# Optimization experiments

Hardware: AMD Instinct MI355X
Metric: run time of the kernel (lower is better)

Reference implementation:

```python
import jax, jax.numpy as jnp
import numpy as np

DIM = 512
NUM_HEADS = 8
HEAD_DIM = DIM // NUM_HEADS
MAX_SLICES = 1024
SCALE = float(np.sqrt(HEAD_DIM))


def setup_inputs() -> dict:
    key = jax.random.key(0)
    ks = jax.random.split(key, 12)
    B, Nv, Nt, D = 4, 1024, 512, DIM
    std = 0.02
    inp = {
        "visual_tokens": jax.random.normal(ks[0], (B, Nv, D), jnp.float32),
        "text_tokens": jax.random.normal(ks[1], (B, Nt, D), jnp.float32),
        # Linear weights stored as [in, out] (i.e., torch W^T), so y = x @ W + b
        "W_Q": jax.random.normal(ks[2], (D, D), jnp.float32) * std,
        "b_Q": jnp.zeros((D,), jnp.float32),
        "W_K": jax.random.normal(ks[3], (D, D), jnp.float32) * std,
        "b_K": jnp.zeros((D,), jnp.float32),
        "W_V": jax.random.normal(ks[4], (D, D), jnp.float32) * std,
        "b_V": jnp.zeros((D,), jnp.float32),
        "W_O": jax.random.normal(ks[5], (D, D), jnp.float32) * std,
        "b_O": jnp.zeros((D,), jnp.float32),
        "bias_table": jax.random.normal(ks[6], (2 * MAX_SLICES - 1, NUM_HEADS), jnp.float32) * std,
        "ln_gamma": jnp.ones((D,), jnp.float32),
        "ln_beta": jnp.zeros((D,), jnp.float32),
    }
    return inp


def _layernorm(x, gamma, beta, eps=1e-5):
    mu = jnp.mean(x, axis=-1, keepdims=True)
    var = jnp.var(x, axis=-1, keepdims=True)
    return (x - mu) * jax.lax.rsqrt(var + eps) * gamma + beta


def reference(visual_tokens, text_tokens, W_Q, b_Q, W_K, b_K, W_V, b_V, W_O, b_O,
              bias_table, ln_gamma, ln_beta):
    Z = jnp.concatenate([visual_tokens, text_tokens], axis=1)  # [B, N, D]
    B, N, D = Z.shape
    Z = _layernorm(Z, ln_gamma, ln_beta)

    def proj(W, b):
        return (Z @ W + b).reshape(B, N, NUM_HEADS, HEAD_DIM).transpose(0, 2, 1, 3)

    Q = proj(W_Q, b_Q)  # [B, H, N, hd]
    K = proj(W_K, b_K)
    V = proj(W_V, b_V)

    attn = jnp.einsum("bhqd,bhkd->bhqk", Q, K) / SCALE  # [B, H, N, N]

    # relative slice bias: [H, N, N]
    coords = jnp.arange(N)
    rel = coords[:, None] - coords[None, :] + (MAX_SLICES - 1)
    rel = jnp.clip(rel, 0, 2 * MAX_SLICES - 2)
    bias = bias_table[rel]                      # [N, N, H]
    bias = jnp.transpose(bias, (2, 0, 1))[None]  # [1, H, N, N]

    attn = jax.nn.softmax(attn + bias, axis=-1)
    out = jnp.einsum("bhqk,bhkd->bhqd", attn, V)  # [B, H, N, hd]
    out = out.transpose(0, 2, 1, 3).reshape(B, N, D)
    return out @ W_O + b_O
```

## Files before the change

### kernel.cpp

```cpp
#include <hip/hip_runtime.h>
#include <stdint.h>

#define NSEQ   1536
#define NBATCH 4
#define NM     (NBATCH * NSEQ)
#define DMODEL 512
#define NHEAD  8
#define HD     64
#define TBLN   2047

typedef __attribute__((ext_vector_type(4))) float  f32x4;
typedef __attribute__((ext_vector_type(4))) int    i32x4;
typedef __attribute__((ext_vector_type(8))) __bf16 bf16x8;
typedef unsigned short u16;

static_assert(sizeof(bf16x8) == 16, "bf16x8 must be 16B");

__device__ inline u16 f2bf(float f) {
  union { float f; uint32_t u; } v; v.f = f;
  uint32_t u = v.u;
  return (u16)((u + 0x7fffu + ((u >> 16) & 1u)) >> 16);
}

__device__ inline bf16x8 ld_bf8(const u16* p) {
  i32x4 v = *(const i32x4*)p;
  return __builtin_bit_cast(bf16x8, v);
}

__device__ inline f32x4 mfma16(bf16x8 a, bf16x8 b, f32x4 c) {
  return __builtin_amdgcn_mfma_f32_16x16x32_bf16(a, b, c, 0, 0, 0);
}

__device__ inline void gload_lds16(const void* g, void* l) {
  __builtin_amdgcn_global_load_lds(
      (__attribute__((address_space(1))) void*)(g),
      (__attribute__((address_space(3))) void*)(l), 16, 0, 0);
}

__device__ inline uint32_t pkbf(float a, float b) {
  uint32_t r;
  asm("v_cvt_pk_bf16_f32 %0, %1, %2" : "=v"(r) : "v"(a), "v"(b));
  return r;
}

__device__ inline float exp2_raw(float x) {
  float r;
  asm("v_exp_f32 %0, %1" : "=v"(r) : "v"(x));
  return r;
}

__device__ inline float bfhi(uint32_t u) {
  union { uint32_t u; float f; } v; v.u = u & 0xffff0000u; return v.f;
}
__device__ inline float bflo(uint32_t u) {
  union { uint32_t u; float f; } v; v.u = u << 16; return v.f;
}

__global__ __launch_bounds__(256) void ln_kernel(
    const float* __restrict__ vis, const float* __restrict__ txt,
    const float* __restrict__ gamma, const float* __restrict__ beta,
    u16* __restrict__ zn) {
  const int lane = threadIdx.x & 63;
  const int row  = blockIdx.x * 4 + (threadIdx.x >> 6);
  const int b = row / NSEQ, n = row - b * NSEQ;
  const float* src = (n < 1024) ? (vis + ((size_t)b * 1024 + n) * DMODEL)
                                : (txt + ((size_t)b * 512 + (n - 1024)) * DMODEL);
  const float4* s4 = (const float4*)src;
  float4 x0 = s4[lane], x1 = s4[lane + 64];
  float s = x0.x + x0.y + x0.z + x0.w + x1.x + x1.y + x1.z + x1.w;
  float q = x0.x*x0.x + x0.y*x0.y + x0.z*x0.z + x0.w*x0.w
          + x1.x*x1.x + x1.y*x1.y + x1.z*x1.z + x1.w*x1.w;
  #pragma unroll
  for (int m = 1; m < 64; m <<= 1) { s += __shfl_xor(s, m); q += __shfl_xor(q, m); }
  const float mean = s * (1.0f / 512.0f);
  const float var  = q * (1.0f / 512.0f) - mean * mean;
  const float rstd = rsqrtf(var + 1e-5f);
  const float4* g4 = (const float4*)gamma;
  const float4* b4 = (const float4*)beta;
  float4 g0 = g4[lane], g1 = g4[lane + 64], p0 = b4[lane], p1 = b4[lane + 64];
  u16* dst = zn + (size_t)row * DMODEL;
  ushort4 o0, o1;
  o0.x = f2bf((x0.x - mean) * rstd * g0.x + p0.x);
  o0.y = f2bf((x0.y - mean) * rstd * g0.y + p0.y);
  o0.z = f2bf((x0.z - mean) * rstd * g0.z + p0.z);
  o0.w = f2bf((x0.w - mean) * rstd * g0.w + p0.w);
  o1.x = f2bf((x1.x - mean) * rstd * g1.x + p1.x);
  o1.y = f2bf((x1.y - mean) * rstd * g1.y + p1.y);
  o1.z = f2bf((x1.z - mean) * rstd * g1.z + p1.z);
  o1.w = f2bf((x1.w - mean) * rstd * g1.w + p1.w);
  *(ushort4*)(dst + lane * 4)        = o0;
  *(ushort4*)(dst + (lane + 64) * 4) = o1;
}

__global__ __launch_bounds__(256) void wtrans_kernel(
    const float* __restrict__ WQ, const float* __restrict__ WK,
    const float* __restrict__ WV, const float* __restrict__ WO,
    u16* __restrict__ wqkvt, u16* __restrict__ wot) {
  __shared__ float t[32][33];
  const int m = blockIdx.z;
  const float* W = (m == 0) ? WQ : (m == 1) ? WK : (m == 2) ? WV : WO;
  const int n0 = blockIdx.x * 32, k0 = blockIdx.y * 32;
  const int tx = threadIdx.x & 31, ty = threadIdx.x >> 5;
  #pragma unroll
  for (int j = 0; j < 4; ++j)
    t[ty + j * 8][tx] = W[(size_t)(k0 + ty + j * 8) * DMODEL + n0 + tx];
  __syncthreads();
  u16* out = (m < 3) ? (wqkvt + (size_t)m * DMODEL * DMODEL) : wot;
  #pragma unroll
  for (int j = 0; j < 4; ++j)
    out[(size_t)(n0 + ty + j * 8) * DMODEL + k0 + tx] = f2bf(t[tx][ty + j * 8]);
}

__global__ __launch_bounds__(256) void gemm_qkv(
    const u16* __restrict__ A, const u16* __restrict__ Bt,
    const float* __restrict__ bQ, const float* __restrict__ bK, const float* __restrict__ bV,
    u16* __restrict__ Q, u16* __restrict__ Kk, u16* __restrict__ Vt) {
  __shared__ __align__(16) u16 lat[128 * 64];
  __shared__ __align__(16) u16 lbt[96 * 64];
  const int tid = threadIdx.x, lane = tid & 63, w = tid >> 6;
  const int wr = w >> 1, wc = w & 1;
  const int m0 = blockIdx.y * 128, n0 = blockIdx.x * 96;
  f32x4 acc[4][3] = {};
  for (int kt = 0; kt < 8; ++kt) {
    const int k0 = kt * 64;
    #pragma unroll
    for (int i = 0; i < 4; ++i) {
      int ch = tid + 256 * i;
      int row = ch >> 3, pc = ch & 7;
      int kk = k0 + ((pc ^ (row & 7)) << 3);
      gload_lds16(A + (size_t)(m0 + row) * DMODEL + kk, lat + (size_t)ch * 8);
    }
    #pragma unroll
    for (int i = 0; i < 3; ++i) {
      int ch = tid + 256 * i;
      int row = ch >> 3, pc = ch & 7;
      int kk = k0 + ((pc ^ (row & 7)) << 3);
      gload_lds16(Bt + (size_t)(n0 + row) * DMODEL + kk, lbt + (size_t)ch * 8);
    }
    __syncthreads();
    #pragma unroll
    for (int ks = 0; ks < 2; ++ks) {
      bf16x8 af[4], bfr[3];
      const int cc = ks * 4 + (lane >> 4);
      #pragma unroll
      for (int f = 0; f < 4; ++f) {
        int ra = wr * 64 + f * 16 + (lane & 15);
        af[f]  = ld_bf8(lat + ra * 64 + ((cc ^ (ra & 7)) << 3));
      }
      #pragma unroll
      for (int f = 0; f < 3; ++f) {
        int rb = wc * 48 + f * 16 + (lane & 15);
        bfr[f] = ld_bf8(lbt + rb * 64 + ((cc ^ (rb & 7)) << 3));
      }
      #pragma unroll
      for (int fr = 0; fr < 4; ++fr)
        #pragma unroll
        for (int fc = 0; fc < 3; ++fc)
          acc[fr][fc] = mfma16(af[fr], bfr[fc], acc[fr][fc]);
    }
    __syncthreads();
  }
  #pragma unroll
  for (int fr = 0; fr < 4; ++fr) {
    const int mbase = m0 + wr * 64 + fr * 16 + ((lane >> 4) << 2);
    const int b = mbase / NSEQ;
    const int nseq = mbase - b * NSEQ;
    #pragma unroll
    for (int fc = 0; fc < 3; ++fc) {
      const int col = n0 + wc * 48 + fc * 16 + (lane & 15);
      const int which = col >> 9;
      const int cw = col & 511;
      const int h = cw >> 6, d = cw & 63;
      const float bias = (which == 0) ? bQ[cw] : (which == 1) ? bK[cw] : bV[cw];
      if (which < 2) {
        u16* dst = ((which == 0) ? Q : Kk) + ((size_t)(b * NHEAD + h) * NSEQ + nseq) * HD + d;
        #pragma unroll
        for (int r = 0; r < 4; ++r) dst[(size_t)r * HD] = f2bf(acc[fr][fc][r] + bias);
      } else {
        ushort4 pv;
        pv.x = f2bf(acc[fr][fc][0] + bias);
        pv.y = f2bf(acc[fr][fc][1] + bias);
        pv.z = f2bf(acc[fr][fc][2] + bias);
        pv.w = f2bf(acc[fr][fc][3] + bias);
        *(ushort4*)(Vt + ((size_t)(b * NHEAD + h) * HD + d) * NSEQ + nseq) = pv;
      }
    }
  }
}

__global__ __launch_bounds__(256) void gemm_oproj(
    const u16* __restrict__ A, const u16* __restrict__ Bt,
    const float* __restrict__ bO, float* __restrict__ out) {
  __shared__ __align__(16) u16 lat[64 * 64];
  __shared__ __align__(16) u16 lbt[64 * 64];
  const int tid = threadIdx.x, lane = tid & 63, w = tid >> 6;
  const int wr = w >> 1, wc = w & 1;
  const int m0 = blockIdx.y * 64, n0 = blockIdx.x * 64;
  f32x4 acc[2][2] = {};
  for (int kt = 0; kt < 8; ++kt) {
    const int k0 = kt * 64;
    #pragma unroll
    for (int i = 0; i < 2; ++i) {
      int ch = tid + 256 * i;
      int row = ch >> 3, pc = ch & 7;
      int kk = k0 + ((pc ^ (row & 7)) << 3);
      gload_lds16(A  + (size_t)(m0 + row) * DMODEL + kk, lat + (size_t)ch * 8);
      gload_lds16(Bt + (size_t)(n0 + row) * DMODEL + kk, lbt + (size_t)ch * 8);
    }
    __syncthreads();
    #pragma unroll
    for (int ks = 0; ks < 2; ++ks) {
      bf16x8 af[2], bfr[2];
      const int cc = ks * 4 + (lane >> 4);
      #pragma unroll
      for (int f = 0; f < 2; ++f) {
        int ra = wr * 32 + f * 16 + (lane & 15);
        af[f]  = ld_bf8(lat + ra * 64 + ((cc ^ (ra & 7)) << 3));
        int rb = wc * 32 + f * 16 + (lane & 15);
        bfr[f] = ld_bf8(lbt + rb * 64 + ((cc ^ (rb & 7)) << 3));
      }
      #pragma unroll
      for (int fr = 0; fr < 2; ++fr)
        #pragma unroll
        for (int fc = 0; fc < 2; ++fc)
          acc[fr][fc] = mfma16(af[fr], bfr[fc], acc[fr][fc]);
    }
    __syncthreads();
  }
  #pragma unroll
  for (int fr = 0; fr < 2; ++fr) {
    const int mbase = m0 + wr * 32 + fr * 16 + ((lane >> 4) << 2);
    #pragma unroll
    for (int fc = 0; fc < 2; ++fc) {
      const int col = n0 + wc * 32 + fc * 16 + (lane & 15);
      const float bias = bO[col];
      float* dst = out + (size_t)mbase * DMODEL + col;
      #pragma unroll
      for (int r = 0; r < 4; ++r) dst[(size_t)r * DMODEL] = acc[fr][fc][r] + bias;
    }
  }
}

__global__ __launch_bounds__(512, 1) void attn_kernel(
    const u16* __restrict__ Q, const u16* __restrict__ K,
    const u16* __restrict__ Vt, const float* __restrict__ table,
    u16* __restrict__ O) {
  __shared__ __align__(16) char smem[126976];
  u16* rb2k = (u16*)smem;
  const int tid = threadIdx.x, lane = tid & 63, w = tid >> 6;
  const int bid = blockIdx.x;
  const int xcd = bid & 7, idx = bid >> 3;
  const int bh  = xcd * 4 + (idx & 3);
  const int qt  = idx >> 2;
  const int h   = bh & (NHEAD - 1);
  for (int t = tid; t < 2 * 3072; t += 512) {
    const int c = (t >= 3072) ? 1 : 0;
    const int x = t - c * 3072;
    int src = 2558 - (x + c);
    src = src < 0 ? 0 : (src > 2046 ? 2046 : src);
    rb2k[c * 3072 + x] = f2bf(table[(size_t)src * NHEAD + h] * 1.4426950408889634f);
  }

  const int lo16 = lane & 15, g = lane >> 4;
  const int ws = w & 3;
  const int hf = w >> 2;
  const int kbase = hf * 768;
  const int q0 = qt * 192 + ws * 48;
  const u16* Qb = Q  + (size_t)bh * NSEQ * HD;
  const u16* Kb = K  + (size_t)bh * NSEQ * HD;
  const u16* Vb = Vt + (size_t)bh * HD * NSEQ;

  const int tloc = tid & 255, shf = tid >> 8;
  const int skbase = shf * 768;
  u16* kl0 = (u16*)(smem + 12288) + shf * 2 * 4096;
  u16* vl0 = (u16*)(smem + 45056) + shf * 2 * 4096;
#define STAGE(b, k0loc)                                                       \
  do {                                                                        \
    _Pragma("unroll")                                                         \
    for (int i = 0; i < 2; ++i) {                                             \
      int ch = tloc + 256 * i;                                                \
      int row = ch >> 3, pc = ch & 7;                                         \
      int col = (pc ^ (row & 7)) << 3;                                        \
      gload_lds16(Kb + (size_t)(skbase + (k0loc) + row) * HD + col,           \
                  kl0 + (size_t)(b) * 4096 + ch * 8);                         \
      gload_lds16(Vb + (size_t)row * NSEQ + skbase + (k0loc) + col,           \
                  vl0 + (size_t)(b) * 4096 + ch * 8);                         \
    }                                                                         \
  } while (0)

  bf16x8 qf[3][2];
  #pragma unroll
  for (int s = 0; s < 3; ++s)
    #pragma unroll
    for (int kd = 0; kd < 2; ++kd)
      qf[s][kd] = ld_bf8(Qb + (size_t)(q0 + s * 16 + lo16) * HD + kd * 32 + g * 8);

  float l_part[3] = {0.f, 0.f, 0.f};
  f32x4 acc[3][4] = {};

  char* plb = smem + 77824 + w * 6144;
  const int pswz  = (lo16 & 7) << 4;
  const int wbase = lo16 * 128;
  const int rswz  = lo16 & 7;
  const int B   = 1535 - q0 - lo16 + 4 * g - 32;
  const int c2  = B & 1;
  const int dwb = (B - c2) >> 1;
  const uint32_t* rbp32 = (const uint32_t*)(rb2k + c2 * 3072);
  const float c1 = 0.125f * 1.4426950408889634f;

  STAGE(0, 0);
  __syncthreads();
  int cur = 0;

  for (int kt = 0; kt < 12; ++kt) {
    const int kglob = kbase + kt * 64;
    const int nxt = cur ^ 1;
    if (kt < 11) {
      STAGE(nxt, (kt + 1) * 64);
      asm volatile("s_waitcnt vmcnt(4)" ::: "memory");
    } else {
      asm volatile("s_waitcnt vmcnt(0)" ::: "memory");
    }
    __builtin_amdgcn_s_barrier();
    const u16* kb = (u16*)(smem + 12288) + (hf * 2 + cur) * 4096;
    const u16* vb = (u16*)(smem + 45056) + (hf * 2 + cur) * 4096;
    float bvf[6][4];
    #pragma unroll
    for (int j = 0; j < 6; ++j) {
      const uint32_t u0 = rbp32[dwb + (kglob >> 1) + 8 * j];
      const uint32_t u1 = rbp32[dwb + (kglob >> 1) + 8 * j + 1];
      bvf[j][0] = bflo(u0); bvf[j][1] = bfhi(u0);
      bvf[j][2] = bflo(u1); bvf[j][3] = bfhi(u1);
    }
    f32x4 st[3][4] = {};
    __builtin_amdgcn_s_setprio(1);
    #pragma unroll
    for (int kc = 0; kc < 4; ++kc) {
      const int row = kc * 16 + lo16;
      const bf16x8 kf0 = ld_bf8(kb + row * 64 + ((g ^ rswz) << 3));
      const bf16x8 kf1 = ld_bf8(kb + row * 64 + (((4 + g) ^ rswz) << 3));
      #pragma unroll
      for (int s = 0; s < 3; ++s) {
        st[s][kc] = mfma16(kf0, qf[s][0], st[s][kc]);
        st[s][kc] = mfma16(kf1, qf[s][1], st[s][kc]);
      }
    }
    __builtin_amdgcn_s_setprio(0);
    #pragma unroll
    for (int s = 0; s < 3; ++s) {
      char* pls = plb + s * 2048;
      #pragma unroll
      for (int kc = 0; kc < 4; ++kc) {
        #pragma unroll
        for (int r = 0; r < 4; ++r) {
          float p = exp2_raw(__builtin_fmaf(st[s][kc][r], c1, bvf[kc - s + 2][r]));
          st[s][kc][r] = p;
          l_part[s] += p;
        }
        uint2 pr;
        pr.x = pkbf(st[s][kc][0], st[s][kc][1]);
        pr.y = pkbf(st[s][kc][2], st[s][kc][3]);
        *(uint2*)(pls + wbase + ((kc * 32 + g * 8) ^ pswz)) = pr;
      }
    }
    __builtin_amdgcn_s_setprio(1);
    #pragma unroll
    for (int t = 0; t < 2; ++t) {
      bf16x8 pb[3];
      #pragma unroll
      for (int s = 0; s < 3; ++s)
        pb[s] = ld_bf8((const u16*)(plb + s * 2048 + wbase + ((t * 64 + g * 16) ^ pswz)));
      #pragma unroll
      for (int fc = 0; fc < 4; ++fc) {
        const int row = fc * 16 + lo16;
        const bf16x8 vf = ld_bf8(vb + row * 64 + (((t * 4 + g) ^ rswz) << 3));
        #pragma unroll
        for (int s = 0; s < 3; ++s)
          acc[s][fc] = mfma16(vf, pb[s], acc[s][fc]);
      }
    }
    __builtin_amdgcn_s_setprio(0);
    __builtin_amdgcn_s_barrier();
    cur = nxt;
  }
  float* scr = (float*)(smem + 12288);
  if (hf == 1) {
    float* wb = scr + ws * 3264;
    #pragma unroll
    for (int s = 0; s < 3; ++s) {
      #pragma unroll
      for (int fc = 0; fc < 4; ++fc)
        ((f32x4*)wb)[(s * 4 + fc) * 64 + lane] = acc[s][fc];
      wb[3072 + s * 64 + lane] = l_part[s];
    }
  }
  __syncthreads();
  if (hf == 0) {
    const float* rb = scr + ws * 3264;
    #pragma unroll
    for (int s = 0; s < 3; ++s) {
      #pragma unroll
      for (int fc = 0; fc < 4; ++fc)
        acc[s][fc] += ((const f32x4*)rb)[(s * 4 + fc) * 64 + lane];
      l_part[s] += rb[3072 + s * 64 + lane];
    }
    const int b = bh >> 3;
    #pragma unroll
    for (int s = 0; s < 3; ++s) {
      float l_r = l_part[s];
      l_r += __shfl_xor(l_r, 16);
      l_r += __shfl_xor(l_r, 32);
      const float inv = 1.0f / l_r;
      u16* orow = O + ((size_t)(b * NSEQ + q0 + s * 16 + lo16)) * DMODEL + h * HD;
      #pragma unroll
      for (int fc = 0; fc < 4; ++fc) {
        uint2 o4;
        o4.x = pkbf(acc[s][fc][0] * inv, acc[s][fc][1] * inv);
        o4.y = pkbf(acc[s][fc][2] * inv, acc[s][fc][3] * inv);
        *(uint2*)(orow + fc * 16 + g * 4) = o4;
      }
    }
  }
#undef STAGE
}

extern "C" void kernel_launch(void* const* d_in, const int* in_sizes, int n_in,
                              void* d_out, int out_size, void* d_ws, size_t ws_size,
                              hipStream_t stream) {
  const float* vis   = (const float*)d_in[0];
  const float* txt   = (const float*)d_in[1];
  const float* WQ    = (const float*)d_in[2];
  const float* bQ    = (const float*)d_in[3];
  const float* WK    = (const float*)d_in[4];
  const float* bK    = (const float*)d_in[5];
  const float* WV    = (const float*)d_in[6];
  const float* bV    = (const float*)d_in[7];
  const float* WO    = (const float*)d_in[8];
  const float* bO    = (const float*)d_in[9];
  const float* table = (const float*)d_in[10];
  const float* gamma = (const float*)d_in[11];
  const float* beta  = (const float*)d_in[12];
  float* out = (float*)d_out;

  char* p = (char*)d_ws;
  u16* zn    = (u16*)p; p += (size_t)NM * DMODEL * 2;
  u16* wqkvt = (u16*)p; p += (size_t)3 * DMODEL * DMODEL * 2;
  u16* wot   = (u16*)p; p += (size_t)DMODEL * DMODEL * 2;
  u16* q     = (u16*)p; p += (size_t)NM * DMODEL * 2;
  u16* k     = (u16*)p; p += (size_t)NM * DMODEL * 2;
  u16* vt    = (u16*)p; p += (size_t)NM * DMODEL * 2;
  u16* o     = (u16*)p; p += (size_t)NM * DMODEL * 2;

  hipLaunchKernelGGL(ln_kernel, dim3(NM / 4), dim3(256), 0, stream,
                     vis, txt, gamma, beta, zn);
  hipLaunchKernelGGL(wtrans_kernel, dim3(16, 16, 4), dim3(256), 0, stream,
                     WQ, WK, WV, WO, wqkvt, wot);
  hipLaunchKernelGGL(gemm_qkv, dim3(16, 48), dim3(256), 0, stream,
                     zn, wqkvt, bQ, bK, bV, q, k, vt);
  hipLaunchKernelGGL(attn_kernel, dim3(256), dim3(512), 0, stream,
                     q, k, vt, table, o);
  hipLaunchKernelGGL(gemm_oproj, dim3(8, 96), dim3(256), 0, stream,
                     o, wot, bO, out);
}
```

Measured before the change: 82.45 us.

## Switch attention to 32x32 MFMA with register-resident P via permlane swaps

The attention kernel moves from 16x16x32 to 32x32x16 bf16 MFMA tiles, with each warp owning 32 query rows instead of 48. The softmax probabilities stay in registers and are rearranged into the B-operand layout with permlane32 swaps, which drops the per-warp LDS staging buffer for P. The block grows to 12 warps (768 threads) and shared memory shrinks from about 124KB to 76KB. The costs are fewer queries per warp, idle warps during staging, and higher register pressure under the new launch bounds.

```diff
diff --git a/kernel.cpp b/kernel.cpp
--- a/kernel.cpp
+++ b/kernel.cpp
@@ -9,9 +9,11 @@
 #define HD     64
 #define TBLN   2047
 
-typedef __attribute__((ext_vector_type(4))) float  f32x4;
-typedef __attribute__((ext_vector_type(4))) int    i32x4;
-typedef __attribute__((ext_vector_type(8))) __bf16 bf16x8;
+typedef __attribute__((ext_vector_type(4)))  float f32x4;
+typedef __attribute__((ext_vector_type(16))) float f32x16;
+typedef __attribute__((ext_vector_type(4)))  int   i32x4;
+typedef __attribute__((ext_vector_type(2)))  unsigned u32x2;
+typedef __attribute__((ext_vector_type(8)))  __bf16 bf16x8;
 typedef unsigned short u16;
 
 static_assert(sizeof(bf16x8) == 16, "bf16x8 must be 16B");
@@ -31,6 +33,10 @@
   return __builtin_amdgcn_mfma_f32_16x16x32_bf16(a, b, c, 0, 0, 0);
 }
 
+__device__ inline f32x16 mfma32(bf16x8 a, bf16x8 b, f32x16 c) {
+  return __builtin_amdgcn_mfma_f32_32x32x16_bf16(a, b, c, 0, 0, 0);
+}
+
 __device__ inline void gload_lds16(const void* g, void* l) {
   __builtin_amdgcn_global_load_lds(
       (__attribute__((address_space(1))) void*)(g),
@@ -41,6 +47,19 @@
   uint32_t r;
   asm("v_cvt_pk_bf16_f32 %0, %1, %2" : "=v"(r) : "v"(a), "v"(b));
   return r;
+}
+
+__device__ inline void plswap(uint32_t& a, uint32_t& b, int hi) {
+#if __has_builtin(__builtin_amdgcn_permlane32_swap)
+  u32x2 r = __builtin_amdgcn_permlane32_swap(a, b, false, false);
+  a = r[0]; b = r[1];
+#else
+  const uint32_t as = (uint32_t)__shfl_xor((int)a, 32);
+  const uint32_t bs = (uint32_t)__shfl_xor((int)b, 32);
+  const uint32_t na = hi ? bs : a;
+  const uint32_t nb = hi ? b : as;
+  a = na; b = nb;
+#endif
 }
 
 __device__ inline float exp2_raw(float x) {
@@ -241,11 +260,11 @@
   }
 }
 
-__global__ __launch_bounds__(512, 1) void attn_kernel(
+__global__ __launch_bounds__(768, 3) void attn_kernel(
     const u16* __restrict__ Q, const u16* __restrict__ K,
     const u16* __restrict__ Vt, const float* __restrict__ table,
     u16* __restrict__ O) {
-  __shared__ __align__(16) char smem[126976];
+  __shared__ __align__(16) char smem[77824];
   u16* rb2k = (u16*)smem;
   const int tid = threadIdx.x, lane = tid & 63, w = tid >> 6;
   const int bid = blockIdx.x;
@@ -253,7 +272,7 @@
   const int bh  = xcd * 4 + (idx & 3);
   const int qt  = idx >> 2;
   const int h   = bh & (NHEAD - 1);
-  for (int t = tid; t < 2 * 3072; t += 512) {
+  for (int t = tid; t < 2 * 3072; t += 768) {
     const int c = (t >= 3072) ? 1 : 0;
     const int x = t - c * 3072;
     int src = 2558 - (x + c);
@@ -261,50 +280,44 @@
     rb2k[c * 3072 + x] = f2bf(table[(size_t)src * NHEAD + h] * 1.4426950408889634f);
   }
 
-  const int lo16 = lane & 15, g = lane >> 4;
-  const int ws = w & 3;
-  const int hf = w >> 2;
+  const int lo32 = lane & 31, hi = lane >> 5;
+  const int ws = (w < 6) ? w : (w - 6);
+  const int hf = (w < 6) ? 0 : 1;
   const int kbase = hf * 768;
-  const int q0 = qt * 192 + ws * 48;
+  const int q  = qt * 192 + ws * 32 + lo32;
   const u16* Qb = Q  + (size_t)bh * NSEQ * HD;
   const u16* Kb = K  + (size_t)bh * NSEQ * HD;
   const u16* Vb = Vt + (size_t)bh * HD * NSEQ;
 
-  const int tloc = tid & 255, shf = tid >> 8;
-  const int skbase = shf * 768;
-  u16* kl0 = (u16*)(smem + 12288) + shf * 2 * 4096;
-  u16* vl0 = (u16*)(smem + 45056) + shf * 2 * 4096;
+  const int tloc = tid - hf * 384;
+  u16* kl0 = (u16*)(smem + 12288) + hf * 2 * 4096;
+  u16* vl0 = (u16*)(smem + 45056) + hf * 2 * 4096;
 #define STAGE(b, k0loc)                                                       \
-  do {                                                                        \
+  if (tloc < 256) {                                                           \
     _Pragma("unroll")                                                         \
     for (int i = 0; i < 2; ++i) {                                             \
       int ch = tloc + 256 * i;                                                \
       int row = ch >> 3, pc = ch & 7;                                         \
       int col = (pc ^ (row & 7)) << 3;                                        \
-      gload_lds16(Kb + (size_t)(skbase + (k0loc) + row) * HD + col,           \
+      gload_lds16(Kb + (size_t)(kbase + (k0loc) + row) * HD + col,            \
                   kl0 + (size_t)(b) * 4096 + ch * 8);                         \
-      gload_lds16(Vb + (size_t)row * NSEQ + skbase + (k0loc) + col,           \
+      gload_lds16(Vb + (size_t)row * NSEQ + kbase + (k0loc) + col,            \
                   vl0 + (size_t)(b) * 4096 + ch * 8);                         \
     }                                                                         \
-  } while (0)
-
-  bf16x8 qf[3][2];
-  #pragma unroll
-  for (int s = 0; s < 3; ++s)
-    #pragma unroll
-    for (int kd = 0; kd < 2; ++kd)
-      qf[s][kd] = ld_bf8(Qb + (size_t)(q0 + s * 16 + lo16) * HD + kd * 32 + g * 8);
-
-  float l_part[3] = {0.f, 0.f, 0.f};
-  f32x4 acc[3][4] = {};
-
-  char* plb = smem + 77824 + w * 6144;
-  const int pswz  = (lo16 & 7) << 4;
-  const int wbase = lo16 * 128;
-  const int rswz  = lo16 & 7;
-  const int B   = 1535 - q0 - lo16 + 4 * g - 32;
-  const int c2  = B & 1;
-  const int dwb = (B - c2) >> 1;
+  }
+
+  bf16x8 qf[4];
+  #pragma unroll
+  for (int ds = 0; ds < 4; ++ds)
+    qf[ds] = ld_bf8(Qb + (size_t)q * HD + ds * 16 + hi * 8);
+
+  float l_part = 0.f;
+  f32x16 acc[2] = {};
+
+  const int rswz = lo32 & 7;
+  const int T0  = 1535 - q + 4 * hi + kbase;
+  const int c2  = T0 & 1;
+  const int dwb = (T0 - c2) >> 1;
   const uint32_t* rbp32 = (const uint32_t*)(rb2k + c2 * 3072);
   const float c1 = 0.125f * 1.4426950408889634f;
 
@@ -313,7 +326,6 @@
   int cur = 0;
 
   for (int kt = 0; kt < 12; ++kt) {
-    const int kglob = kbase + kt * 64;
     const int nxt = cur ^ 1;
     if (kt < 11) {
       STAGE(nxt, (kt + 1) * 64);
@@ -324,102 +336,93 @@
     __builtin_amdgcn_s_barrier();
     const u16* kb = (u16*)(smem + 12288) + (hf * 2 + cur) * 4096;
     const u16* vb = (u16*)(smem + 45056) + (hf * 2 + cur) * 4096;
-    float bvf[6][4];
-    #pragma unroll
-    for (int j = 0; j < 6; ++j) {
-      const uint32_t u0 = rbp32[dwb + (kglob >> 1) + 8 * j];
-      const uint32_t u1 = rbp32[dwb + (kglob >> 1) + 8 * j + 1];
-      bvf[j][0] = bflo(u0); bvf[j][1] = bfhi(u0);
-      bvf[j][2] = bflo(u1); bvf[j][3] = bfhi(u1);
-    }
-    f32x4 st[3][4] = {};
-    __builtin_amdgcn_s_setprio(1);
-    #pragma unroll
-    for (int kc = 0; kc < 4; ++kc) {
-      const int row = kc * 16 + lo16;
-      const bf16x8 kf0 = ld_bf8(kb + row * 64 + ((g ^ rswz) << 3));
-      const bf16x8 kf1 = ld_bf8(kb + row * 64 + (((4 + g) ^ rswz) << 3));
-      #pragma unroll
-      for (int s = 0; s < 3; ++s) {
-        st[s][kc] = mfma16(kf0, qf[s][0], st[s][kc]);
-        st[s][kc] = mfma16(kf1, qf[s][1], st[s][kc]);
-      }
-    }
-    __builtin_amdgcn_s_setprio(0);
-    #pragma unroll
-    for (int s = 0; s < 3; ++s) {
-      char* pls = plb + s * 2048;
-      #pragma unroll
-      for (int kc = 0; kc < 4; ++kc) {
-        #pragma unroll
-        for (int r = 0; r < 4; ++r) {
-          float p = exp2_raw(__builtin_fmaf(st[s][kc][r], c1, bvf[kc - s + 2][r]));
-          st[s][kc][r] = p;
-          l_part[s] += p;
-        }
-        uint2 pr;
-        pr.x = pkbf(st[s][kc][0], st[s][kc][1]);
-        pr.y = pkbf(st[s][kc][2], st[s][kc][3]);
-        *(uint2*)(pls + wbase + ((kc * 32 + g * 8) ^ pswz)) = pr;
-      }
-    }
-    __builtin_amdgcn_s_setprio(1);
-    #pragma unroll
-    for (int t = 0; t < 2; ++t) {
-      bf16x8 pb[3];
-      #pragma unroll
-      for (int s = 0; s < 3; ++s)
-        pb[s] = ld_bf8((const u16*)(plb + s * 2048 + wbase + ((t * 64 + g * 16) ^ pswz)));
-      #pragma unroll
-      for (int fc = 0; fc < 4; ++fc) {
-        const int row = fc * 16 + lo16;
-        const bf16x8 vf = ld_bf8(vb + row * 64 + (((t * 4 + g) ^ rswz) << 3));
-        #pragma unroll
-        for (int s = 0; s < 3; ++s)
-          acc[s][fc] = mfma16(vf, pb[s], acc[s][fc]);
-      }
-    }
-    __builtin_amdgcn_s_setprio(0);
+    #pragma unroll
+    for (int ktile = 0; ktile < 2; ++ktile) {
+      f32x16 st = {};
+      __builtin_amdgcn_s_setprio(1);
+      #pragma unroll
+      for (int ds = 0; ds < 4; ++ds) {
+        const int row = ktile * 32 + lo32;
+        const bf16x8 kf = ld_bf8(kb + row * 64 + (((2 * ds + hi) ^ rswz) << 3));
+        st = mfma32(kf, qf[ds], st);
+      }
+      __builtin_amdgcn_s_setprio(0);
+      const int dwk = dwb + ((kt * 64 + ktile * 32) >> 1);
+      float bv[4][4];
+      #pragma unroll
+      for (int gp = 0; gp < 4; ++gp) {
+        const uint32_t u0 = rbp32[dwk + 4 * gp];
+        const uint32_t u1 = rbp32[dwk + 4 * gp + 1];
+        bv[gp][0] = bflo(u0); bv[gp][1] = bfhi(u0);
+        bv[gp][2] = bflo(u1); bv[gp][3] = bfhi(u1);
+      }
+      #pragma unroll
+      for (int r = 0; r < 16; ++r) {
+        float p = exp2_raw(__builtin_fmaf(st[r], c1, bv[r >> 2][r & 3]));
+        st[r] = p;
+        l_part += p;
+      }
+      uint32_t wv[8];
+      #pragma unroll
+      for (int i = 0; i < 8; ++i) wv[i] = pkbf(st[2 * i], st[2 * i + 1]);
+      plswap(wv[0], wv[2], hi);  plswap(wv[1], wv[3], hi);
+      plswap(wv[4], wv[6], hi);  plswap(wv[5], wv[7], hi);
+      i32x4 b0; b0[0] = (int)wv[0]; b0[1] = (int)wv[1]; b0[2] = (int)wv[2]; b0[3] = (int)wv[3];
+      i32x4 b1; b1[0] = (int)wv[4]; b1[1] = (int)wv[5]; b1[2] = (int)wv[6]; b1[3] = (int)wv[7];
+      const bf16x8 pb0 = __builtin_bit_cast(bf16x8, b0);
+      const bf16x8 pb1 = __builtin_bit_cast(bf16x8, b1);
+      __builtin_amdgcn_s_setprio(1);
+      #pragma unroll
+      for (int dh = 0; dh < 2; ++dh) {
+        const int vrow = dh * 32 + lo32;
+        const bf16x8 va0 = ld_bf8(vb + vrow * 64 + (((4 * ktile + 0 + hi) ^ rswz) << 3));
+        acc[dh] = mfma32(va0, pb0, acc[dh]);
+        const bf16x8 va1 = ld_bf8(vb + vrow * 64 + (((4 * ktile + 2 + hi) ^ rswz) << 3));
+        acc[dh] = mfma32(va1, pb1, acc[dh]);
+      }
+      __builtin_amdgcn_s_setprio(0);
+    }
     __builtin_amdgcn_s_barrier();
     cur = nxt;
   }
   float* scr = (float*)(smem + 12288);
   if (hf == 1) {
-    float* wb = scr + ws * 3264;
-    #pragma unroll
-    for (int s = 0; s < 3; ++s) {
-      #pragma unroll
-      for (int fc = 0; fc < 4; ++fc)
-        ((f32x4*)wb)[(s * 4 + fc) * 64 + lane] = acc[s][fc];
-      wb[3072 + s * 64 + lane] = l_part[s];
-    }
+    float* wb = scr + ws * 2112;
+    #pragma unroll
+    for (int dh = 0; dh < 2; ++dh)
+      #pragma unroll
+      for (int i = 0; i < 4; ++i) {
+        f32x4 c4; c4[0] = acc[dh][4*i]; c4[1] = acc[dh][4*i+1];
+        c4[2] = acc[dh][4*i+2]; c4[3] = acc[dh][4*i+3];
+        ((f32x4*)wb)[(dh * 4 + i) * 64 + lane] = c4;
+      }
+    wb[2048 + lane] = l_part;
   }
   __syncthreads();
   if (hf == 0) {
-    const float* rb = scr + ws * 3264;
-    #pragma unroll
-    for (int s = 0; s < 3; ++s) {
-      #pragma unroll
-      for (int fc = 0; fc < 4; ++fc)
-        acc[s][fc] += ((const f32x4*)rb)[(s * 4 + fc) * 64 + lane];
-      l_part[s] += rb[3072 + s * 64 + lane];
-    }
+    const float* rb = scr + ws * 2112;
+    #pragma unroll
+    for (int dh = 0; dh < 2; ++dh)
+      #pragma unroll
+      for (int i = 0; i < 4; ++i) {
+        const f32x4 c4 = ((const f32x4*)rb)[(dh * 4 + i) * 64 + lane];
+        acc[dh][4*i] += c4[0]; acc[dh][4*i+1] += c4[1];
+        acc[dh][4*i+2] += c4[2]; acc[dh][4*i+3] += c4[3];
+      }
+    l_part += rb[2048 + lane];
+    float l_r = l_part + __shfl_xor(l_part, 32);
+    const float inv = 1.0f / l_r;
     const int b = bh >> 3;
-    #pragma unroll
-    for (int s = 0; s < 3; ++s) {
-      float l_r = l_part[s];
-      l_r += __shfl_xor(l_r, 16);
-      l_r += __shfl_xor(l_r, 32);
-      const float inv = 1.0f / l_r;
-      u16* orow = O + ((size_t)(b * NSEQ + q0 + s * 16 + lo16)) * DMODEL + h * HD;
-      #pragma unroll
-      for (int fc = 0; fc < 4; ++fc) {
+    u16* orow = O + ((size_t)(b * NSEQ + q)) * DMODEL + h * HD;
+    #pragma unroll
+    for (int dh = 0; dh < 2; ++dh)
+      #pragma unroll
+      for (int gp = 0; gp < 4; ++gp) {
         uint2 o4;
-        o4.x = pkbf(acc[s][fc][0] * inv, acc[s][fc][1] * inv);
-        o4.y = pkbf(acc[s][fc][2] * inv, acc[s][fc][3] * inv);
-        *(uint2*)(orow + fc * 16 + g * 4) = o4;
-      }
-    }
+        o4.x = pkbf(acc[dh][4*gp]   * inv, acc[dh][4*gp+1] * inv);
+        o4.y = pkbf(acc[dh][4*gp+2] * inv, acc[dh][4*gp+3] * inv);
+        *(uint2*)(orow + dh * 32 + 8 * gp + 4 * hi) = o4;
+      }
   }
 #undef STAGE
 }
@@ -457,7 +460,7 @@
                      WQ, WK, WV, WO, wqkvt, wot);
   hipLaunchKernelGGL(gemm_qkv, dim3(16, 48), dim3(256), 0, stream,
                      zn, wqkvt, bQ, bK, bV, q, k, vt);
-  hipLaunchKernelGGL(attn_kernel, dim3(256), dim3(512), 0, stream,
+  hipLaunchKernelGGL(attn_kernel, dim3(256), dim3(768), 0, stream,
                      q, k, vt, table, o);
   hipLaunchKernelGGL(gemm_oproj, dim3(8, 96), dim3(256), 0, stream,
                      o, wot, bO, out);
```

After: 81.99 us. About the same (-0.5%).
